# Performance work log

Measured on AMD Instinct MI355X. Metric: run time of the kernel, lower is better.

Reference implementation:

```python
import jax, jax.numpy as jnp
import numpy as np

B, N, D, L = 64, 512, 256, 4


def setup_inputs() -> dict:
    key = jax.random.key(0)
    ks = jax.random.split(key, 10)
    scale = 1.0 / np.sqrt(D)
    x = jax.random.normal(ks[0], (B, N, D), dtype=jnp.float32)
    adj = (jax.random.uniform(ks[1], (B, N, N)) < 0.1).astype(jnp.float32)
    return {
        "x": x,
        "adj": adj,
        "w_attn_w": jax.random.normal(ks[2], (L, D, D), dtype=jnp.float32) * scale,
        "w_attn_b": jnp.zeros((L, D), dtype=jnp.float32),
        "lin0_w": jax.random.normal(ks[3], (L, D, D), dtype=jnp.float32) * scale,
        "lin0_b": jnp.zeros((L, D), dtype=jnp.float32),
        "lin1_w": jax.random.normal(ks[4], (L, D, D), dtype=jnp.float32) * scale,
        "lin1_b": jnp.zeros((L, D), dtype=jnp.float32),
        "final_w": jax.random.normal(ks[5], (D, D), dtype=jnp.float32) * scale,
        "final_b": jnp.zeros((D,), dtype=jnp.float32),
    }


def reference(x, adj, w_attn_w, w_attn_b, lin0_w, lin0_b, lin1_w, lin1_b, final_w, final_b):
    # set self-loops on the adjacency diagonal (in-place in the torch code)
    idx = jnp.arange(N)
    adj = adj.at[:, idx, idx].set(1.0)
    eye = 1e-5 * jnp.eye(N, dtype=x.dtype)
    attls = []
    for l in range(L):
        x0 = x
        # q = w_attn[l](x): torch Linear is x @ W.T + b, W: [out,in]
        q = jnp.einsum('bnd,od->bno', x, w_attn_w[l]) + w_attn_b[l]
        adj_attn = jax.nn.sigmoid(jnp.einsum('bij,bkj->bik', q, x))  # [B,N,N]
        adj_attn = (adj_attn + eye) * adj
        adj_attn = adj_attn / jnp.sum(adj_attn, axis=-1, keepdims=True)
        attls.append(adj_attn)
        x = jnp.einsum('bij,bjd->bid', adj_attn, x)
        x = jax.nn.relu(jnp.einsum('bnd,od->bno', x, lin0_w[l]) + lin0_b[l])
        x = jax.nn.relu(jnp.einsum('bnd,od->bno', x, lin1_w[l]) + lin1_b[l])
        x = x + x0
    x = jnp.einsum('bnd,od->bno', x, final_w) + final_b
    return (x, jnp.stack(attls))
```

## Files before the change

### kernel.cpp

```cpp
#include <hip/hip_runtime.h>
#include <cstdint>

#define B_ 64
#define N_ 512
#define D_ 256
#define L_ 4

typedef __bf16 bf16;
typedef __attribute__((ext_vector_type(8))) __bf16 bf16x8;
typedef __attribute__((ext_vector_type(4))) __bf16 bf16x4;
typedef __attribute__((ext_vector_type(4))) float f32x4;

#define MFMA16(a, b, c) __builtin_amdgcn_mfma_f32_16x16x32_bf16((a), (b), (c), 0, 0, 0)

__device__ __forceinline__ float sigmoidf_(float z) {
  return 1.0f / (1.0f + __expf(-z));
}


#define UIDX(u) (((size_t)(u)) * 64 + lane)

__global__ __launch_bounds__(256) void pack_w(
    const float* __restrict__ src, bf16* __restrict__ dst)
{
  const int tid = threadIdx.x, lane = tid & 63;
  const int U = blockIdx.x * 4 + (tid >> 6);
  const int m = U >> 7, u = U & 127;
  const int r16 = u >> 3, kc = u & 7;
  const int row = r16 * 16 + (lane & 15);
  const int k0 = kc * 32 + (lane >> 4) * 8;
  const float* s = src + (size_t)m * D_ * D_ + (size_t)row * D_ + k0;
  const float4 v0 = *(const float4*)s;
  const float4 v1 = *(const float4*)(s + 4);
  bf16x8 o;
  o[0] = (bf16)v0.x; o[1] = (bf16)v0.y; o[2] = (bf16)v0.z; o[3] = (bf16)v0.w;
  o[4] = (bf16)v1.x; o[5] = (bf16)v1.y; o[6] = (bf16)v1.z; o[7] = (bf16)v1.w;
  ((bf16x8*)dst)[(size_t)U * 64 + lane] = o;
}

__global__ __launch_bounds__(256) void init_pack(
    const float* __restrict__ x, bf16* __restrict__ xbpk, bf16* __restrict__ xTpk)
{
  const int tid = threadIdx.x, lane = tid & 63;
  const int U = blockIdx.x * 4 + (tid >> 6);
  const int b = U >> 9, u = U & 511;
  if (u < 256) {
    const int n = (u >> 3) * 16 + (lane & 15);
    const int d = (u & 7) * 32 + (lane >> 4) * 8;
    const float* s = x + ((size_t)(b * N_ + n)) * D_ + d;
    const float4 v0 = *(const float4*)s;
    const float4 v1 = *(const float4*)(s + 4);
    bf16x8 o;
    o[0] = (bf16)v0.x; o[1] = (bf16)v0.y; o[2] = (bf16)v0.z; o[3] = (bf16)v0.w;
    o[4] = (bf16)v1.x; o[5] = (bf16)v1.y; o[6] = (bf16)v1.z; o[7] = (bf16)v1.w;
    ((bf16x8*)xbpk)[((size_t)b * 256 + u) * 64 + lane] = o;
  } else {
    const int u2 = u - 256;
    const int d = (u2 >> 4) * 16 + (lane & 15);
    const int n = (u2 & 15) * 32 + (lane >> 4) * 8;
    bf16x8 o;
#pragma unroll
    for (int e = 0; e < 8; ++e)
      o[e] = (bf16)x[((size_t)(b * N_ + n + e)) * D_ + d];
    ((bf16x8*)xTpk)[((size_t)b * 256 + u2) * 64 + lane] = o;
  }
}

__global__ __launch_bounds__(256, 3) void gat_layer(
    const bf16* __restrict__ xbpk_in, const bf16* __restrict__ xTpk_in,
    bf16* __restrict__ xbpk_out, bf16* __restrict__ xTpk_out,
    const bf16* __restrict__ Wap, const float* __restrict__ ba,
    const bf16* __restrict__ W0p, const float* __restrict__ b0,
    const bf16* __restrict__ W1p, const float* __restrict__ b1,
    const float* __restrict__ adj, const unsigned short* __restrict__ bits_in,
    unsigned short* __restrict__ bits_out, float* __restrict__ outA)
{
  __shared__ bf16 qs[32 * 264];
  __shared__ bf16 xps[32 * 520];
  __shared__ float psum[4][32];
  __shared__ float rinvs[32];
  __shared__ unsigned int bits_s[512];

  const int tid = threadIdx.x, w = tid >> 6, lane = tid & 63;
  const int l16 = lane & 15, quad = lane >> 4;
  const int wg = blockIdx.x;
  const int lid = (wg & 7) * 128 + (wg >> 3);
  const int b = lid >> 4;
  const int row0 = (lid & 15) * 32;

  const bf16x8* Xbp = (const bf16x8*)xbpk_in + (size_t)b * 16384;
  const bf16x8* Xtp = (const bf16x8*)xTpk_in + (size_t)b * 16384;
  bf16x8* XbpO = (bf16x8*)xbpk_out + (size_t)b * 16384;
  bf16x8* XtpO = (bf16x8*)xTpk_out + (size_t)b * 16384;
  const bf16x8* Wa8 = (const bf16x8*)Wap;
  const bf16x8* W08 = (const bf16x8*)W0p;
  const bf16x8* W18 = (const bf16x8*)W1p;

  if (bits_in) {
#pragma unroll
    for (int e = 0; e < 2; ++e) {
      const int t = tid + e * 256;
      bits_s[t] = ((const unsigned int*)bits_in)[((size_t)b * N_ + row0) * 16 + t];
    }
  }

  {
    f32x4 acc0[2][4] = {};
#pragma unroll
    for (int ks = 0; ks < 8; ++ks) {
      bf16x8 af[2];
#pragma unroll
      for (int m = 0; m < 2; ++m)
        af[m] = Xbp[UIDX(((row0 >> 4) + m) * 8 + ks)];
      bf16x8 bw[4];
#pragma unroll
      for (int i = 0; i < 4; ++i)
        bw[i] = Wa8[UIDX((4 * w + i) * 8 + ks)];
#pragma unroll
      for (int m = 0; m < 2; ++m)
#pragma unroll
        for (int i = 0; i < 4; ++i) acc0[m][i] = MFMA16(af[m], bw[i], acc0[m][i]);
    }
#pragma unroll
    for (int m = 0; m < 2; ++m)
#pragma unroll
      for (int i = 0; i < 4; ++i) {
        const int col = 64 * w + 16 * i + l16;
        const float bv = ba[col];
#pragma unroll
        for (int r = 0; r < 4; ++r)
          qs[(16 * m + quad * 4 + r) * 264 + col] = (bf16)(acc0[m][i][r] + bv);
      }
  }
  __syncthreads();

  float p[2][4] = {};
  bf16x8 afc[8][2];
#pragma unroll
  for (int ks = 0; ks < 8; ++ks)
#pragma unroll
    for (int m = 0; m < 2; ++m)
      afc[ks][m] = *(const bf16x8*)&qs[(16 * m + l16) * 264 + ks * 32 + quad * 8];

  for (int ct = 0; ct < 4; ++ct) {
    f32x4 acc1[2][2] = {};
#pragma unroll
    for (int ks = 0; ks < 8; ++ks) {
      bf16x8 bx[2];
#pragma unroll
      for (int jt = 0; jt < 2; ++jt)
        bx[jt] = Xbp[UIDX((ct * 8 + w * 2 + jt) * 8 + ks)];
#pragma unroll
      for (int m = 0; m < 2; ++m)
#pragma unroll
        for (int jt = 0; jt < 2; ++jt)
          acc1[m][jt] = MFMA16(afc[ks][m], bx[jt], acc1[m][jt]);
    }
#pragma unroll
    for (int jt = 0; jt < 2; ++jt) {
      const int lcol = ct * 128 + w * 32 + jt * 16 + l16;
      const int piece = ct * 8 + w * 2 + jt;
#pragma unroll
      for (int m = 0; m < 2; ++m)
#pragma unroll
        for (int r = 0; r < 4; ++r) {
          const int row = 16 * m + quad * 4 + r;
          const int grow = row0 + row;
          float av;
          if (bits_in) {
            const unsigned short m16 = ((const unsigned short*)bits_s)[row * 32 + piece];
            av = (float)((m16 >> l16) & 1);
          } else {
            av = __builtin_nontemporal_load(
                adj + ((size_t)b * N_ + grow) * N_ + lcol);
          }
          const bool diag = (grow == lcol);
          if (bits_out) {
            const unsigned long long bal = __ballot(diag || av != 0.0f);
            if (l16 == 0)
              bits_out[((size_t)b * N_ + row0 + 16 * m + 4 * quad + r) * 32 + piece] =
                  (unsigned short)((bal >> (quad * 16)) & 0xFFFFull);
          }
          const float sg = sigmoidf_(acc1[m][jt][r]);
          const float v = diag ? (sg + 1e-5f) : sg * av;
          const bf16 bv = (bf16)v;
          xps[row * 520 + lcol] = bv;
          p[m][r] += (float)bv;
        }
    }
  }
#pragma unroll
  for (int m = 0; m < 2; ++m)
#pragma unroll
    for (int r = 0; r < 4; ++r) {
#pragma unroll
      for (int msk = 1; msk < 16; msk <<= 1) p[m][r] += __shfl_xor(p[m][r], msk, 64);
    }
  if (l16 == 0) {
#pragma unroll
    for (int m = 0; m < 2; ++m)
#pragma unroll
      for (int r = 0; r < 4; ++r) psum[w][16 * m + quad * 4 + r] = p[m][r];
  }
  __syncthreads();
  if (tid < 32)
    rinvs[tid] = 1.0f / (psum[0][tid] + psum[1][tid] + psum[2][tid] + psum[3][tid]);
  __syncthreads();

  const size_t abase = ((size_t)b * N_ + row0) * N_;
#pragma unroll
  for (int e = 0; e < 16; ++e) {
    const int idx = tid + e * 256;
    const int row = idx >> 7, c4 = (idx & 127) * 4;
    const float ri = rinvs[row];
    bf16x4 pv = *(const bf16x4*)&xps[row * 520 + c4];
    f32x4 nv;
    nv[0] = (float)pv[0] * ri; nv[1] = (float)pv[1] * ri;
    nv[2] = (float)pv[2] * ri; nv[3] = (float)pv[3] * ri;
    __builtin_nontemporal_store(nv, (f32x4*)(outA + abase + (size_t)row * N_ + c4));
    bf16x4 o;
    o[0] = (bf16)nv[0]; o[1] = (bf16)nv[1]; o[2] = (bf16)nv[2]; o[3] = (bf16)nv[3];
    *(bf16x4*)&xps[row * 520 + c4] = o;
  }
  __syncthreads();

  {
    f32x4 acc3[2][4] = {};
#pragma unroll
    for (int ks = 0; ks < 16; ++ks) {
      bf16x8 af[2];
#pragma unroll
      for (int m = 0; m < 2; ++m)
        af[m] = *(const bf16x8*)&xps[(16 * m + l16) * 520 + ks * 32 + quad * 8];
      bf16x8 bt[4];
#pragma unroll
      for (int i = 0; i < 4; ++i)
        bt[i] = Xtp[UIDX((4 * w + i) * 16 + ks)];
#pragma unroll
      for (int m = 0; m < 2; ++m)
#pragma unroll
        for (int i = 0; i < 4; ++i) acc3[m][i] = MFMA16(af[m], bt[i], acc3[m][i]);
    }
#pragma unroll
    for (int m = 0; m < 2; ++m)
#pragma unroll
      for (int i = 0; i < 4; ++i) {
        const int d = 64 * w + 16 * i + l16;
#pragma unroll
        for (int r = 0; r < 4; ++r)
          qs[(16 * m + quad * 4 + r) * 264 + d] = (bf16)acc3[m][i][r];
      }
  }
  __syncthreads();

  {
    f32x4 acc[2][4] = {};
#pragma unroll
    for (int ks = 0; ks < 8; ++ks) {
      bf16x8 af[2];
#pragma unroll
      for (int m = 0; m < 2; ++m)
        af[m] = *(const bf16x8*)&qs[(16 * m + l16) * 264 + ks * 32 + quad * 8];
      bf16x8 bw[4];
#pragma unroll
      for (int i = 0; i < 4; ++i)
        bw[i] = W08[UIDX((4 * w + i) * 8 + ks)];
#pragma unroll
      for (int m = 0; m < 2; ++m)
#pragma unroll
        for (int i = 0; i < 4; ++i) acc[m][i] = MFMA16(af[m], bw[i], acc[m][i]);
    }
#pragma unroll
    for (int m = 0; m < 2; ++m)
#pragma unroll
      for (int i = 0; i < 4; ++i) {
        const int col = 64 * w + 16 * i + l16;
        const float bv = b0[col];
#pragma unroll
        for (int r = 0; r < 4; ++r)
          xps[(16 * m + quad * 4 + r) * 264 + col] = (bf16)fmaxf(acc[m][i][r] + bv, 0.0f);
      }
  }
  __syncthreads();

  {
    bf16x8 ah[8][2];
#pragma unroll
    for (int ks = 0; ks < 8; ++ks)
#pragma unroll
      for (int m = 0; m < 2; ++m)
        ah[ks][m] = *(const bf16x8*)&xps[(16 * m + l16) * 264 + ks * 32 + quad * 8];
#pragma unroll
    for (int j = 0; j < 4; ++j) {
      const int t = w * 4 + j;
      const bf16x8 v = Xbp[UIDX(((row0 >> 4) + (t >> 3)) * 8 + (t & 7))];
      const int nl = (t >> 3) * 16 + l16, dd = (t & 7) * 32 + quad * 8;
      *(bf16x8*)&qs[nl * 264 + dd] = v;
    }
    __syncthreads();

    f32x4 acc[2][4] = {};
#pragma unroll
    for (int ks = 0; ks < 8; ++ks) {
      bf16x8 bw[4];
#pragma unroll
      for (int i = 0; i < 4; ++i)
        bw[i] = W18[UIDX((4 * w + i) * 8 + ks)];
#pragma unroll
      for (int m = 0; m < 2; ++m)
#pragma unroll
        for (int i = 0; i < 4; ++i) acc[m][i] = MFMA16(ah[ks][m], bw[i], acc[m][i]);
    }
#pragma unroll
    for (int m = 0; m < 2; ++m)
#pragma unroll
      for (int i = 0; i < 4; ++i) {
        const int d = 64 * w + 16 * i + l16;
        const float bv = b1[d];
#pragma unroll
        for (int r = 0; r < 4; ++r) {
          const int nl = 16 * m + quad * 4 + r;
          const float x0 = (float)qs[nl * 264 + d];
          const float t2 = fmaxf(acc[m][i][r] + bv, 0.0f) + x0;
          xps[nl * 264 + d] = (bf16)t2;
        }
      }
    __syncthreads();

#pragma unroll
    for (int j = 0; j < 4; ++j) {
      const int t = w * 4 + j;
      const int nl = (t >> 3) * 16 + l16, dd = (t & 7) * 32 + quad * 8;
      const bf16x8 v = *(const bf16x8*)&xps[nl * 264 + dd];
      XbpO[UIDX(((row0 >> 4) + (t >> 3)) * 8 + (t & 7))] = v;
    }
#pragma unroll
    for (int j = 0; j < 4; ++j) {
      const int t = w * 4 + j;
      const int dd = t * 16 + l16;
      bf16x8 v;
#pragma unroll
      for (int e = 0; e < 8; ++e)
        v[e] = xps[(quad * 8 + e) * 264 + dd];
      XtpO[UIDX(t * 16 + (row0 >> 5))] = v;
    }
  }
}

__global__ __launch_bounds__(256, 4) void final_proj(
    const bf16* __restrict__ xbpk, const bf16* __restrict__ Wfp,
    const float* __restrict__ bfv, float* __restrict__ outX)
{
  const int tid = threadIdx.x, w = tid >> 6, lane = tid & 63;
  const int l16 = lane & 15, quad = lane >> 4;
  const int wg = blockIdx.x;
  const int lid = (wg & 7) * 128 + (wg >> 3);
  const int row0g = lid * 32;
  const int b = row0g >> 9, n0 = row0g & 511;
  const bf16x8* Xbp = (const bf16x8*)xbpk + (size_t)b * 16384;
  const bf16x8* Wf8 = (const bf16x8*)Wfp;
  f32x4 acc[2][4] = {};
#pragma unroll
  for (int ks = 0; ks < 8; ++ks) {
    bf16x8 af[2];
#pragma unroll
    for (int m = 0; m < 2; ++m)
      af[m] = Xbp[UIDX(((n0 >> 4) + m) * 8 + ks)];
    bf16x8 bw[4];
#pragma unroll
    for (int i = 0; i < 4; ++i)
      bw[i] = Wf8[UIDX((4 * w + i) * 8 + ks)];
#pragma unroll
    for (int m = 0; m < 2; ++m)
#pragma unroll
      for (int i = 0; i < 4; ++i) acc[m][i] = MFMA16(af[m], bw[i], acc[m][i]);
  }
#pragma unroll
  for (int m = 0; m < 2; ++m)
#pragma unroll
    for (int i = 0; i < 4; ++i) {
      const int col = 64 * w + 16 * i + l16;
      const float bv = bfv[col];
#pragma unroll
      for (int r = 0; r < 4; ++r) {
        const size_t R = (size_t)row0g + 16 * m + quad * 4 + r;
        __builtin_nontemporal_store(acc[m][i][r] + bv, outX + R * D_ + col);
      }
    }
}

extern "C" void kernel_launch(void* const* d_in, const int* in_sizes, int n_in,
                              void* d_out, int out_size, void* d_ws, size_t ws_size,
                              hipStream_t stream)
{
  const float* x_in  = (const float*)d_in[0];
  const float* adj   = (const float*)d_in[1];
  const float* wattn = (const float*)d_in[2];
  const float* battn = (const float*)d_in[3];
  const float* w0    = (const float*)d_in[4];
  const float* b0    = (const float*)d_in[5];
  const float* w1    = (const float*)d_in[6];
  const float* b1    = (const float*)d_in[7];
  const float* wf    = (const float*)d_in[8];
  const float* bfin  = (const float*)d_in[9];

  float* out_x    = (float*)d_out;
  float* out_attn = out_x + (size_t)B_ * N_ * D_;

  const size_t XBN = (size_t)B_ * N_ * D_;
  const int DD2 = D_ * D_;
  bf16* wb   = (bf16*)d_ws;
  bf16* xbp0 = wb + 13 * DD2;
  bf16* xtp0 = xbp0 + XBN;
  bf16* xbp1 = xtp0 + XBN;
  bf16* xtp1 = xbp1 + XBN;
  unsigned short* bits = (unsigned short*)(xtp1 + XBN);

  pack_w<<<dim3(4 * 32), 256, 0, stream>>>(wattn, wb);
  pack_w<<<dim3(4 * 32), 256, 0, stream>>>(w0, wb + 4 * DD2);
  pack_w<<<dim3(4 * 32), 256, 0, stream>>>(w1, wb + 8 * DD2);
  pack_w<<<dim3(1 * 32), 256, 0, stream>>>(wf, wb + 12 * DD2);

  init_pack<<<dim3(8192), 256, 0, stream>>>(x_in, xbp0, xtp0);

  bf16* xbps[2] = {xbp0, xbp1};
  bf16* xtps[2] = {xtp0, xtp1};
  for (int l = 0; l < L_; ++l) {
    const int pi = l & 1, po = 1 - pi;
    gat_layer<<<dim3((N_ / 32) * B_), 256, 0, stream>>>(
        xbps[pi], xtps[pi], xbps[po], xtps[po],
        wb + l * DD2, battn + l * D_,
        wb + (4 + l) * DD2, b0 + l * D_,
        wb + (8 + l) * DD2, b1 + l * D_,
        adj, (l == 0) ? nullptr : bits, (l == 0) ? bits : nullptr,
        out_attn + (size_t)l * B_ * N_ * N_);
  }
  final_proj<<<dim3((B_ * N_) / 32), 256, 0, stream>>>(
      xbps[0], wb + 12 * DD2, bfin, out_x);
}
```

Measured before the change: 792.8 us.

## Enlarge gat_layer tile to 64 rows with 512-thread blocks

Each workgroup now processes 64 node rows with 8 waves instead of 32 rows with 4 waves. The per-wave MFMA tiling across all stages is reshaped: Q·Xᵀ is done in a single pass over 512 columns instead of four column chunks, and the other GEMMs split output columns across 8 waves. This is meant to halve how often the shared weights and per-batch X operands are re-read from global memory. In exchange it roughly doubles LDS use to about 104KB per block and limits occupancy to one block per CU, which may hurt latency hiding.

```diff
diff --git a/kernel.cpp b/kernel.cpp
--- a/kernel.cpp
+++ b/kernel.cpp
@@ -66,7 +66,7 @@
   }
 }
 
-__global__ __launch_bounds__(256, 3) void gat_layer(
+__global__ __launch_bounds__(512, 1) void gat_layer(
     const bf16* __restrict__ xbpk_in, const bf16* __restrict__ xTpk_in,
     bf16* __restrict__ xbpk_out, bf16* __restrict__ xTpk_out,
     const bf16* __restrict__ Wap, const float* __restrict__ ba,
@@ -75,18 +75,18 @@
     const float* __restrict__ adj, const unsigned short* __restrict__ bits_in,
     unsigned short* __restrict__ bits_out, float* __restrict__ outA)
 {
-  __shared__ bf16 qs[32 * 264];
-  __shared__ bf16 xps[32 * 520];
-  __shared__ float psum[4][32];
-  __shared__ float rinvs[32];
-  __shared__ unsigned int bits_s[512];
+  __shared__ bf16 qs[64 * 264];
+  __shared__ bf16 xps[64 * 520];
+  __shared__ float psum[8][64];
+  __shared__ float rinvs[64];
+  __shared__ unsigned int bits_s[1024];
 
   const int tid = threadIdx.x, w = tid >> 6, lane = tid & 63;
   const int l16 = lane & 15, quad = lane >> 4;
   const int wg = blockIdx.x;
-  const int lid = (wg & 7) * 128 + (wg >> 3);
-  const int b = lid >> 4;
-  const int row0 = (lid & 15) * 32;
+  const int lid = (wg & 7) * 64 + (wg >> 3);
+  const int b = lid >> 3;
+  const int row0 = (lid & 7) * 64;
 
   const bf16x8* Xbp = (const bf16x8*)xbpk_in + (size_t)b * 16384;
   const bf16x8* Xtp = (const bf16x8*)xTpk_in + (size_t)b * 16384;
@@ -99,33 +99,33 @@
   if (bits_in) {
 #pragma unroll
     for (int e = 0; e < 2; ++e) {
-      const int t = tid + e * 256;
+      const int t = tid + e * 512;
       bits_s[t] = ((const unsigned int*)bits_in)[((size_t)b * N_ + row0) * 16 + t];
     }
   }
 
   {
-    f32x4 acc0[2][4] = {};
+    f32x4 acc0[4][2] = {};
 #pragma unroll
     for (int ks = 0; ks < 8; ++ks) {
-      bf16x8 af[2];
-#pragma unroll
-      for (int m = 0; m < 2; ++m)
+      bf16x8 af[4];
+#pragma unroll
+      for (int m = 0; m < 4; ++m)
         af[m] = Xbp[UIDX(((row0 >> 4) + m) * 8 + ks)];
-      bf16x8 bw[4];
-#pragma unroll
-      for (int i = 0; i < 4; ++i)
-        bw[i] = Wa8[UIDX((4 * w + i) * 8 + ks)];
-#pragma unroll
-      for (int m = 0; m < 2; ++m)
-#pragma unroll
-        for (int i = 0; i < 4; ++i) acc0[m][i] = MFMA16(af[m], bw[i], acc0[m][i]);
-    }
-#pragma unroll
-    for (int m = 0; m < 2; ++m)
-#pragma unroll
-      for (int i = 0; i < 4; ++i) {
-        const int col = 64 * w + 16 * i + l16;
+      bf16x8 bw[2];
+#pragma unroll
+      for (int i = 0; i < 2; ++i)
+        bw[i] = Wa8[UIDX((2 * w + i) * 8 + ks)];
+#pragma unroll
+      for (int m = 0; m < 4; ++m)
+#pragma unroll
+        for (int i = 0; i < 2; ++i) acc0[m][i] = MFMA16(af[m], bw[i], acc0[m][i]);
+    }
+#pragma unroll
+    for (int m = 0; m < 4; ++m)
+#pragma unroll
+      for (int i = 0; i < 2; ++i) {
+        const int col = 32 * w + 16 * i + l16;
         const float bv = ba[col];
 #pragma unroll
         for (int r = 0; r < 4; ++r)
@@ -134,34 +134,31 @@
   }
   __syncthreads();
 
-  float p[2][4] = {};
-  bf16x8 afc[8][2];
-#pragma unroll
-  for (int ks = 0; ks < 8; ++ks)
-#pragma unroll
-    for (int m = 0; m < 2; ++m)
-      afc[ks][m] = *(const bf16x8*)&qs[(16 * m + l16) * 264 + ks * 32 + quad * 8];
-
-  for (int ct = 0; ct < 4; ++ct) {
-    f32x4 acc1[2][2] = {};
+  float p[4][4] = {};
+  {
+    f32x4 acc1[4][4] = {};
 #pragma unroll
     for (int ks = 0; ks < 8; ++ks) {
-      bf16x8 bx[2];
-#pragma unroll
-      for (int jt = 0; jt < 2; ++jt)
-        bx[jt] = Xbp[UIDX((ct * 8 + w * 2 + jt) * 8 + ks)];
-#pragma unroll
-      for (int m = 0; m < 2; ++m)
-#pragma unroll
-        for (int jt = 0; jt < 2; ++jt)
-          acc1[m][jt] = MFMA16(afc[ks][m], bx[jt], acc1[m][jt]);
-    }
-#pragma unroll
-    for (int jt = 0; jt < 2; ++jt) {
-      const int lcol = ct * 128 + w * 32 + jt * 16 + l16;
-      const int piece = ct * 8 + w * 2 + jt;
-#pragma unroll
-      for (int m = 0; m < 2; ++m)
+      bf16x8 af[4];
+#pragma unroll
+      for (int m = 0; m < 4; ++m)
+        af[m] = *(const bf16x8*)&qs[(16 * m + l16) * 264 + ks * 32 + quad * 8];
+      bf16x8 bx[4];
+#pragma unroll
+      for (int jt = 0; jt < 4; ++jt)
+        bx[jt] = Xbp[UIDX((4 * w + jt) * 8 + ks)];
+#pragma unroll
+      for (int m = 0; m < 4; ++m)
+#pragma unroll
+        for (int jt = 0; jt < 4; ++jt)
+          acc1[m][jt] = MFMA16(af[m], bx[jt], acc1[m][jt]);
+    }
+#pragma unroll
+    for (int jt = 0; jt < 4; ++jt) {
+      const int lcol = 64 * w + jt * 16 + l16;
+      const int piece = 4 * w + jt;
+#pragma unroll
+      for (int m = 0; m < 4; ++m)
 #pragma unroll
         for (int r = 0; r < 4; ++r) {
           const int row = 16 * m + quad * 4 + r;
@@ -190,7 +187,7 @@
     }
   }
 #pragma unroll
-  for (int m = 0; m < 2; ++m)
+  for (int m = 0; m < 4; ++m)
 #pragma unroll
     for (int r = 0; r < 4; ++r) {
 #pragma unroll
@@ -198,19 +195,23 @@
     }
   if (l16 == 0) {
 #pragma unroll
-    for (int m = 0; m < 2; ++m)
+    for (int m = 0; m < 4; ++m)
 #pragma unroll
       for (int r = 0; r < 4; ++r) psum[w][16 * m + quad * 4 + r] = p[m][r];
   }
   __syncthreads();
-  if (tid < 32)
-    rinvs[tid] = 1.0f / (psum[0][tid] + psum[1][tid] + psum[2][tid] + psum[3][tid]);
+  if (tid < 64) {
+    float s = 0.0f;
+#pragma unroll
+    for (int ww = 0; ww < 8; ++ww) s += psum[ww][tid];
+    rinvs[tid] = 1.0f / s;
+  }
   __syncthreads();
 
   const size_t abase = ((size_t)b * N_ + row0) * N_;
 #pragma unroll
   for (int e = 0; e < 16; ++e) {
-    const int idx = tid + e * 256;
+    const int idx = tid + e * 512;
     const int row = idx >> 7, c4 = (idx & 127) * 4;
     const float ri = rinvs[row];
     bf16x4 pv = *(const bf16x4*)&xps[row * 520 + c4];
@@ -225,27 +226,27 @@
   __syncthreads();
 
   {
-    f32x4 acc3[2][4] = {};
+    f32x4 acc3[4][2] = {};
 #pragma unroll
     for (int ks = 0; ks < 16; ++ks) {
-      bf16x8 af[2];
-#pragma unroll
-      for (int m = 0; m < 2; ++m)
+      bf16x8 af[4];
+#pragma unroll
+      for (int m = 0; m < 4; ++m)
         af[m] = *(const bf16x8*)&xps[(16 * m + l16) * 520 + ks * 32 + quad * 8];
-      bf16x8 bt[4];
-#pragma unroll
-      for (int i = 0; i < 4; ++i)
-        bt[i] = Xtp[UIDX((4 * w + i) * 16 + ks)];
-#pragma unroll
-      for (int m = 0; m < 2; ++m)
-#pragma unroll
-        for (int i = 0; i < 4; ++i) acc3[m][i] = MFMA16(af[m], bt[i], acc3[m][i]);
-    }
-#pragma unroll
-    for (int m = 0; m < 2; ++m)
-#pragma unroll
-      for (int i = 0; i < 4; ++i) {
-        const int d = 64 * w + 16 * i + l16;
+      bf16x8 bt[2];
+#pragma unroll
+      for (int i = 0; i < 2; ++i)
+        bt[i] = Xtp[UIDX((2 * w + i) * 16 + ks)];
+#pragma unroll
+      for (int m = 0; m < 4; ++m)
+#pragma unroll
+        for (int i = 0; i < 2; ++i) acc3[m][i] = MFMA16(af[m], bt[i], acc3[m][i]);
+    }
+#pragma unroll
+    for (int m = 0; m < 4; ++m)
+#pragma unroll
+      for (int i = 0; i < 2; ++i) {
+        const int d = 32 * w + 16 * i + l16;
 #pragma unroll
         for (int r = 0; r < 4; ++r)
           qs[(16 * m + quad * 4 + r) * 264 + d] = (bf16)acc3[m][i][r];
@@ -254,27 +255,27 @@
   __syncthreads();
 
   {
-    f32x4 acc[2][4] = {};
+    f32x4 acc[4][2] = {};
 #pragma unroll
     for (int ks = 0; ks < 8; ++ks) {
-      bf16x8 af[2];
-#pragma unroll
-      for (int m = 0; m < 2; ++m)
+      bf16x8 af[4];
+#pragma unroll
+      for (int m = 0; m < 4; ++m)
         af[m] = *(const bf16x8*)&qs[(16 * m + l16) * 264 + ks * 32 + quad * 8];
-      bf16x8 bw[4];
-#pragma unroll
-      for (int i = 0; i < 4; ++i)
-        bw[i] = W08[UIDX((4 * w + i) * 8 + ks)];
-#pragma unroll
-      for (int m = 0; m < 2; ++m)
-#pragma unroll
-        for (int i = 0; i < 4; ++i) acc[m][i] = MFMA16(af[m], bw[i], acc[m][i]);
-    }
-#pragma unroll
-    for (int m = 0; m < 2; ++m)
-#pragma unroll
-      for (int i = 0; i < 4; ++i) {
-        const int col = 64 * w + 16 * i + l16;
+      bf16x8 bw[2];
+#pragma unroll
+      for (int i = 0; i < 2; ++i)
+        bw[i] = W08[UIDX((2 * w + i) * 8 + ks)];
+#pragma unroll
+      for (int m = 0; m < 4; ++m)
+#pragma unroll
+        for (int i = 0; i < 2; ++i) acc[m][i] = MFMA16(af[m], bw[i], acc[m][i]);
+    }
+#pragma unroll
+    for (int m = 0; m < 4; ++m)
+#pragma unroll
+      for (int i = 0; i < 2; ++i) {
+        const int col = 32 * w + 16 * i + l16;
         const float bv = b0[col];
 #pragma unroll
         for (int r = 0; r < 4; ++r)
@@ -284,65 +285,64 @@
   __syncthreads();
 
   {
-    bf16x8 ah[8][2];
-#pragma unroll
-    for (int ks = 0; ks < 8; ++ks)
-#pragma unroll
-      for (int m = 0; m < 2; ++m)
-        ah[ks][m] = *(const bf16x8*)&xps[(16 * m + l16) * 264 + ks * 32 + quad * 8];
 #pragma unroll
     for (int j = 0; j < 4; ++j) {
-      const int t = w * 4 + j;
-      const bf16x8 v = Xbp[UIDX(((row0 >> 4) + (t >> 3)) * 8 + (t & 7))];
-      const int nl = (t >> 3) * 16 + l16, dd = (t & 7) * 32 + quad * 8;
-      *(bf16x8*)&qs[nl * 264 + dd] = v;
+      const int uu = w * 4 + j;
+      const int rr = uu >> 3, kc = uu & 7;
+      const bf16x8 v = Xbp[UIDX(((row0 >> 4) + rr) * 8 + kc)];
+      *(bf16x8*)&qs[(rr * 16 + l16) * 264 + kc * 32 + quad * 8] = v;
+    }
+    f32x4 acc[4][2] = {};
+#pragma unroll
+    for (int ks = 0; ks < 8; ++ks) {
+      bf16x8 af[4];
+#pragma unroll
+      for (int m = 0; m < 4; ++m)
+        af[m] = *(const bf16x8*)&xps[(16 * m + l16) * 264 + ks * 32 + quad * 8];
+      bf16x8 bw[2];
+#pragma unroll
+      for (int i = 0; i < 2; ++i)
+        bw[i] = W18[UIDX((2 * w + i) * 8 + ks)];
+#pragma unroll
+      for (int m = 0; m < 4; ++m)
+#pragma unroll
+        for (int i = 0; i < 2; ++i) acc[m][i] = MFMA16(af[m], bw[i], acc[m][i]);
     }
     __syncthreads();
 
-    f32x4 acc[2][4] = {};
-#pragma unroll
-    for (int ks = 0; ks < 8; ++ks) {
-      bf16x8 bw[4];
-#pragma unroll
-      for (int i = 0; i < 4; ++i)
-        bw[i] = W18[UIDX((4 * w + i) * 8 + ks)];
-#pragma unroll
-      for (int m = 0; m < 2; ++m)
-#pragma unroll
-        for (int i = 0; i < 4; ++i) acc[m][i] = MFMA16(ah[ks][m], bw[i], acc[m][i]);
-    }
-#pragma unroll
-    for (int m = 0; m < 2; ++m)
-#pragma unroll
-      for (int i = 0; i < 4; ++i) {
-        const int d = 64 * w + 16 * i + l16;
+#pragma unroll
+    for (int m = 0; m < 4; ++m)
+#pragma unroll
+      for (int i = 0; i < 2; ++i) {
+        const int d = 32 * w + 16 * i + l16;
         const float bv = b1[d];
 #pragma unroll
         for (int r = 0; r < 4; ++r) {
           const int nl = 16 * m + quad * 4 + r;
           const float x0 = (float)qs[nl * 264 + d];
           const float t2 = fmaxf(acc[m][i][r] + bv, 0.0f) + x0;
-          xps[nl * 264 + d] = (bf16)t2;
+          qs[nl * 264 + d] = (bf16)t2;
         }
       }
     __syncthreads();
 
 #pragma unroll
     for (int j = 0; j < 4; ++j) {
-      const int t = w * 4 + j;
-      const int nl = (t >> 3) * 16 + l16, dd = (t & 7) * 32 + quad * 8;
-      const bf16x8 v = *(const bf16x8*)&xps[nl * 264 + dd];
-      XbpO[UIDX(((row0 >> 4) + (t >> 3)) * 8 + (t & 7))] = v;
+      const int uu = w * 4 + j;
+      const int rr = uu >> 3, kc = uu & 7;
+      const bf16x8 v = *(const bf16x8*)&qs[(rr * 16 + l16) * 264 + kc * 32 + quad * 8];
+      XbpO[UIDX(((row0 >> 4) + rr) * 8 + kc)] = v;
     }
 #pragma unroll
     for (int j = 0; j < 4; ++j) {
-      const int t = w * 4 + j;
-      const int dd = t * 16 + l16;
+      const int uu = w * 4 + j;
+      const int d16 = uu >> 1, nk = uu & 1;
+      const int d = d16 * 16 + l16;
       bf16x8 v;
 #pragma unroll
       for (int e = 0; e < 8; ++e)
-        v[e] = xps[(quad * 8 + e) * 264 + dd];
-      XtpO[UIDX(t * 16 + (row0 >> 5))] = v;
+        v[e] = qs[(nk * 32 + quad * 8 + e) * 264 + d];
+      XtpO[UIDX(d16 * 16 + (row0 >> 5) + nk)] = v;
     }
   }
 }
@@ -427,7 +427,7 @@
   bf16* xtps[2] = {xtp0, xtp1};
   for (int l = 0; l < L_; ++l) {
     const int pi = l & 1, po = 1 - pi;
-    gat_layer<<<dim3((N_ / 32) * B_), 256, 0, stream>>>(
+    gat_layer<<<dim3((N_ / 64) * B_), 512, 0, stream>>>(
         xbps[pi], xtps[pi], xbps[po], xtps[po],
         wb + l * DD2, battn + l * D_,
         wb + (4 + l) * DD2, b0 + l * D_,
```

New measurement: 725.0 us. -8.5%, faster.
